# Performance work log

Hardware: AMD Instinct MI355X
Metric: run time of the kernel (lower is better)

## Reference

```python
import jax, jax.numpy as jnp
import numpy as np

# Flax OptimizedLSTMCell gate order: i, f, g, o

def _lstm_step(c, h, x, W_ih, W_hh, b):
    z = x @ W_ih + h @ W_hh + b          # [B, 4H]
    i, f, g, o = jnp.split(z, 4, axis=-1)
    i = jax.nn.sigmoid(i)
    f = jax.nn.sigmoid(f)
    g = jnp.tanh(g)
    o = jax.nn.sigmoid(o)
    c = f * c + i * g
    h = o * jnp.tanh(c)
    return c, h


def setup_inputs() -> dict:
    key = jax.random.key(0)
    ks = jax.random.split(key, 5)
    B, Tw, Ta, F_AUTO, O, H = 1024, 512, 512, 24, 8, 256
    F = F_AUTO + O  # warmup feature dim must equal auto features + output dim
    return {
        "c0": jnp.zeros((B, H), jnp.float32),
        "h0": jnp.zeros((B, H), jnp.float32),
        "warmup_input": jax.random.normal(ks[0], (B, Tw, F), jnp.float32),
        "auto_input": jax.random.normal(ks[1], (B, Ta, F_AUTO), jnp.float32),
        "W_ih": jax.random.normal(ks[2], (F, 4 * H), jnp.float32) * (1.0 / np.sqrt(F)),
        "W_hh": jax.random.normal(ks[3], (H, 4 * H), jnp.float32) * (1.0 / np.sqrt(H)),
        "b": jnp.zeros((4 * H,), jnp.float32),
        "W_out": jax.random.normal(ks[4], (H, O), jnp.float32) * (1.0 / np.sqrt(H)),
        "b_out": jnp.zeros((O,), jnp.float32),
    }


def reference(c0, h0, warmup_input, auto_input, W_ih, W_hh, b, W_out, b_out):
    # ---- warmup phase: plain LSTM scan over warmup_input ----
    def warm_step(carry, x_t):
        c, h = carry
        c, h = _lstm_step(c, h, x_t, W_ih, W_hh, b)
        return (c, h), h

    xs_w = jnp.swapaxes(warmup_input, 0, 1)            # [Tw, B, F] time-major
    (c, h), hs = jax.lax.scan(warm_step, (c0, h0), xs_w)
    warm_h = jnp.swapaxes(hs, 0, 1)                    # [B, Tw, H]
    output_warm = warm_h @ W_out + b_out               # [B, Tw, O]
    y_last = output_warm[:, -1]                        # [B, O]

    def auto_step(carry, x_t):
        c, h, y = carry
        in_x = jnp.concatenate([x_t, y], axis=-1)      # [B, F_auto + O] == [B, F]
        c, h = _lstm_step(c, h, in_x, W_ih, W_hh, b)
        y = h @ W_out + b_out
        return (c, h, y), y

    xs_a = jnp.swapaxes(auto_input, 0, 1)              # [Ta, B, F_auto]
    _, ys = jax.lax.scan(auto_step, (c, h, y_last), xs_a)
    rest_output = jnp.swapaxes(ys, 0, 1)               # [B, Ta, O]

    return jnp.concatenate([output_warm, rest_output], axis=-2)  # [B, Tw+Ta, O]
```

## Files before the change

kernel.cpp:

```cpp
#include <hip/hip_runtime.h>
#include <stdint.h>


#define B_TOTAL   1024
#define H_DIM     256
#define F_WARM    32
#define F_AUTO    24
#define O_DIM     8
#define T_WARM    512
#define T_TOTAL   1024
#define N4H       1024
#define A_STR     104

typedef __attribute__((ext_vector_type(8))) short short8;
typedef __attribute__((ext_vector_type(4))) float float4v;

#define GLOBAL_AS __attribute__((address_space(1)))
#define LDS_AS    __attribute__((address_space(3)))
#define XSCOPE    __HIP_MEMORY_SCOPE_AGENT

__device__ __forceinline__ short f2bf(float x) {
    union { float f; uint32_t u; } v; v.f = x;
    uint32_t r = v.u + 0x7FFFu + ((v.u >> 16) & 1u);
    return (short)(r >> 16);
}
__device__ __forceinline__ float sigmoid_(float x) {
    const float e = __expf(-x);
    return __builtin_amdgcn_rcpf(1.0f + e);
}
__device__ __forceinline__ float tanh_(float x) {
    const float e = __expf(-2.0f * fabsf(x));
    const float t = (1.0f - e) * __builtin_amdgcn_rcpf(1.0f + e);
    return x >= 0.0f ? t : -t;
}
__device__ __forceinline__ uint32_t uc_ld(const uint32_t* p) {
    return __hip_atomic_load(p, __ATOMIC_RELAXED, XSCOPE);
}
__device__ __forceinline__ void uc_st(uint32_t* p, uint32_t v) {
    __hip_atomic_store(p, v, __ATOMIC_RELAXED, XSCOPE);
}

__global__ __launch_bounds__(256, 1)
void lstm_q4(const float* __restrict__ c0, const float* __restrict__ h0,
             const float* __restrict__ warm, const float* __restrict__ autoin,
             const float* __restrict__ W_ih, const float* __restrict__ W_hh,
             const float* __restrict__ bvec, const float* __restrict__ W_out,
             const float* __restrict__ b_out, float* __restrict__ out,
             unsigned short* __restrict__ ws)
{
    const int tid  = threadIdx.x;
    const int w    = tid >> 6;
    const int l    = tid & 63;
    const int n16  = l & 15;
    const int kg   = l >> 4;
    const int bid  = blockIdx.x;
    const int tile = bid & 63;
    const int q    = bid >> 6;
    const int row0 = tile * 16;
    const int hcol = q * 64 + w * 16 + n16;
    const int cl   = w * 16 + n16;

    const int pb0 = ((q + 1) & 3) * 64 + tile;
    const int pb1 = ((q + 2) & 3) * 64 + tile;
    const int pb2 = ((q + 3) & 3) * 64 + tile;

    uint32_t* myflag = (uint32_t*)((char*)ws + (size_t)bid * 64);
    const uint32_t* pf0 = (const uint32_t*)((char*)ws + (size_t)pb0 * 64);
    const uint32_t* pf1 = (const uint32_t*)((char*)ws + (size_t)pb1 * 64);
    const uint32_t* pf2 = (const uint32_t*)((char*)ws + (size_t)pb2 * 64);
    uint32_t* xbase = (uint32_t*)((char*)ws + 16384);
    uint32_t*       obuf = xbase + (size_t)bid * 1024;
    const uint32_t* pd0  = xbase + (size_t)pb0 * 1024;
    const uint32_t* pd1  = xbase + (size_t)pb1 * 1024;
    const uint32_t* pd2  = xbase + (size_t)pb2 * 1024;

    __shared__ __align__(16) short Abuf[2][16 * A_STR];
    __shared__ __align__(16) unsigned short wsWl[4096];
    __shared__ float biasL[256];
    __shared__ __align__(16) float xstage[512];

    for (int idx = tid; idx < 4096; idx += 256) {
        const int i = idx & 7, lane = (idx >> 3) & 63, kk = idx >> 9;
        const int k = kk * 32 + (lane >> 4) * 8 + i;
        const int n = lane & 15;
        wsWl[idx] = (unsigned short)((n < O_DIM) ? f2bf(W_out[k * O_DIM + n]) : (short)0);
    }
    {
        const int g = tid >> 6, loc = tid & 63;
        biasL[tid] = bvec[g * 256 + q * 64 + loc];
    }

    short8 bwx[4];
    short8 bwo[2][4];
    short8 bwhp[3][2][4];
    #pragma unroll
    for (int g = 0; g < 4; ++g) {
        const int col = g * 256 + hcol;
        {
            short8 f;
            #pragma unroll
            for (int i = 0; i < 8; ++i)
                f[i] = f2bf(W_ih[(kg * 8 + i) * N4H + col]);
            bwx[g] = f;
        }
        #pragma unroll
        for (int lc = 0; lc < 2; ++lc) {
            short8 f;
            #pragma unroll
            for (int i = 0; i < 8; ++i)
                f[i] = f2bf(W_hh[(q * 64 + lc * 32 + kg * 8 + i) * N4H + col]);
            bwo[lc][g] = f;
        }
        #pragma unroll
        for (int pi = 0; pi < 3; ++pi) {
            const int qq = (q + 1 + pi) & 3;
            #pragma unroll
            for (int lc = 0; lc < 2; ++lc) {
                short8 f;
                #pragma unroll
                for (int i = 0; i < 8; ++i)
                    f[i] = f2bf(W_hh[(qq * 64 + lc * 32 + kg * 8 + i) * N4H + col]);
                bwhp[pi][lc][g] = f;
            }
        }
    }

    const float bout = (w == 0 && n16 < O_DIM) ? b_out[n16] : 0.0f;

    float creg[4];
    #pragma unroll
    for (int r = 0; r < 4; ++r)
        creg[r] = c0[(size_t)(row0 + kg * 4 + r) * H_DIM + hcol];

    #pragma unroll
    for (int e = 0; e < 2; ++e) {
        const int idx = tid + e * 256;
        const int r = idx >> 5, cx = idx & 31;
        Abuf[0][r * A_STR + cx] =
            f2bf(warm[(size_t)(row0 + r) * (T_WARM * F_WARM) + cx]);
    }
    #pragma unroll
    for (int e = 0; e < 4; ++e) {
        const int idx = tid + e * 256;
        const int r = idx >> 6, c = idx & 63;
        Abuf[0][r * A_STR + F_WARM + c] =
            f2bf(h0[(size_t)(row0 + r) * H_DIM + q * 64 + c]);
    }
    short8 phf[3][2];
    #pragma unroll
    for (int pi = 0; pi < 3; ++pi) {
        const int qq = (q + 1 + pi) & 3;
        #pragma unroll
        for (int lc = 0; lc < 2; ++lc) {
            short8 f;
            #pragma unroll
            for (int i = 0; i < 8; ++i)
                f[i] = f2bf(h0[(size_t)(row0 + n16) * H_DIM
                               + qq * 64 + lc * 32 + kg * 8 + i]);
            phf[pi][lc] = f;
        }
    }

    __syncthreads();
    float bb[4];
    #pragma unroll
    for (int g = 0; g < 4; ++g) bb[g] = biasL[g * 64 + cl];

    const int aoff = n16 * A_STR + kg * 8;
    short* curp = &Abuf[0][0];
    short* nxtp = &Abuf[1][0];
    const short8* wsW8 = (const short8*)wsWl;
    const int shx = (n16 & 1) * 16;

    for (int t = 0; t < T_TOTAL; ++t) {
        __syncthreads();

        if (tid == 0)
            uc_st(myflag, (uint32_t)t);

        uint32_t fv0 = 0, fv1 = 0, fv2 = 0;
        if (t >= 1) { fv0 = uc_ld(pf0); fv1 = uc_ld(pf1); fv2 = uc_ld(pf2); }

        const int tn = t + 1;
        if (tn < T_TOTAL) {
            #pragma unroll
            for (int e = 0; e < 2; ++e) {
                const int idx = tid + e * 256;
                const int r = idx >> 5, cx = idx & 31;
                const float* gp;
                if (tn < T_WARM)
                    gp = &warm[(size_t)(row0 + r) * (T_WARM * F_WARM)
                               + (size_t)tn * F_WARM + cx];
                else
                    gp = &autoin[(size_t)(row0 + r) * (T_WARM * F_AUTO)
                                 + (size_t)(tn - T_WARM) * F_AUTO
                                 + ((cx < F_AUTO) ? cx : 0)];
                __builtin_amdgcn_global_load_lds(
                    (const GLOBAL_AS void*)gp,
                    (LDS_AS void*)&xstage[e * 256 + w * 64], 4, 0, 0);
            }
        }

        const short* ab = curp + aoff;
        short8 afh[2];
        #pragma unroll
        for (int lc = 0; lc < 2; ++lc)
            afh[lc] = *(const short8*)(ab + 32 + lc * 32);

        float4v acc[4];
        #pragma unroll
        for (int g = 0; g < 4; ++g)
            acc[g] = (float4v){0.f, 0.f, 0.f, 0.f};
        #pragma unroll
        for (int lc = 0; lc < 2; ++lc)
            #pragma unroll
            for (int g = 0; g < 4; ++g)
                acc[g] = __builtin_amdgcn_mfma_f32_16x16x32_bf16(
                             afh[lc], bwo[lc][g], acc[g], 0, 0, 0);

        if (t < T_WARM) {
            const short8 af = *(const short8*)(ab);
            #pragma unroll
            for (int g = 0; g < 4; ++g)
                acc[g] = __builtin_amdgcn_mfma_f32_16x16x32_bf16(
                             af, bwx[g], acc[g], 0, 0, 0);
        }

        if (t >= 1) {
            const uint32_t want = (uint32_t)t;
            while (fv0 < want || fv1 < want || fv2 < want) {
                __builtin_amdgcn_s_sleep(1);
                fv0 = uc_ld(pf0); fv1 = uc_ld(pf1); fv2 = uc_ld(pf2);
            }
            asm volatile("" ::: "memory");
            const int slot = ((t - 1) & 1) * 512;
            #pragma unroll
            for (int pi = 0; pi < 3; ++pi) {
                const uint32_t* pd = (pi == 0) ? pd0 : (pi == 1) ? pd1 : pd2;
                #pragma unroll
                for (int lc = 0; lc < 2; ++lc) {
                    uint32_t wv[8];
                    #pragma unroll
                    for (int i = 0; i < 8; ++i)
                        wv[i] = uc_ld(&pd[slot + (lc * 32 + kg * 8 + i) * 8 + (n16 >> 1)]);
                    short8 f;
                    #pragma unroll
                    for (int i = 0; i < 8; ++i)
                        f[i] = (short)((wv[i] >> shx) & 0xFFFFu);
                    phf[pi][lc] = f;
                }
            }
        }

        #pragma unroll
        for (int pi = 0; pi < 3; ++pi)
            #pragma unroll
            for (int lc = 0; lc < 2; ++lc)
                #pragma unroll
                for (int g = 0; g < 4; ++g)
                    acc[g] = __builtin_amdgcn_mfma_f32_16x16x32_bf16(
                                 phf[pi][lc], bwhp[pi][lc][g], acc[g], 0, 0, 0);

        if (w == 0 && t >= 1 && (q == 0 || t >= T_WARM)) {
            float4v ya = (float4v){bout, bout, bout, bout};
            #pragma unroll
            for (int lc = 0; lc < 2; ++lc)
                ya = __builtin_amdgcn_mfma_f32_16x16x32_bf16(
                         afh[lc], wsW8[(q * 2 + lc) * 64 + l], ya, 0, 0, 0);
            #pragma unroll
            for (int pi = 0; pi < 3; ++pi) {
                const int qq = (q + 1 + pi) & 3;
                #pragma unroll
                for (int lc = 0; lc < 2; ++lc)
                    ya = __builtin_amdgcn_mfma_f32_16x16x32_bf16(
                             phf[pi][lc], wsW8[(qq * 2 + lc) * 64 + l], ya, 0, 0, 0);
            }
            if (n16 < O_DIM) {
                if (q == 0) {
                    #pragma unroll
                    for (int r = 0; r < 4; ++r)
                        out[(size_t)(row0 + kg * 4 + r) * (T_TOTAL * O_DIM)
                            + (size_t)(t - 1) * O_DIM + n16] = ya[r];
                }
                if (t >= T_WARM) {
                    #pragma unroll
                    for (int r = 0; r < 4; ++r)
                        curp[(kg * 4 + r) * A_STR + F_AUTO + n16] = f2bf(ya[r]);
                }
            }
        }

        if (t >= T_WARM) {
            __syncthreads();
            const short8 af = *(const short8*)(ab);
            #pragma unroll
            for (int g = 0; g < 4; ++g)
                acc[g] = __builtin_amdgcn_mfma_f32_16x16x32_bf16(
                             af, bwx[g], acc[g], 0, 0, 0);
        }

        uint32_t hp[2];
        {
            float hv0, hv1, hv2, hv3;
            #pragma unroll
            for (int r = 0; r < 4; ++r) {
                const float ig = sigmoid_(acc[0][r] + bb[0]);
                const float fg = sigmoid_(acc[1][r] + bb[1]);
                const float gg = tanh_(acc[2][r] + bb[2]);
                const float og = sigmoid_(acc[3][r] + bb[3]);
                const float cc = fg * creg[r] + ig * gg;
                creg[r] = cc;
                const float hh = og * tanh_(cc);
                if (r == 0) hv0 = hh; else if (r == 1) hv1 = hh;
                else if (r == 2) hv2 = hh; else hv3 = hh;
            }
            uint32_t u0, u1;
            asm("v_cvt_pk_bf16_f32 %0, %1, %2" : "=v"(u0) : "v"(hv0), "v"(hv1));
            asm("v_cvt_pk_bf16_f32 %0, %1, %2" : "=v"(u1) : "v"(hv2), "v"(hv3));
            hp[0] = u0; hp[1] = u1;
        }

        asm volatile("s_waitcnt vmcnt(0)" ::: "memory");

        if (tn < T_TOTAL) {
            #pragma unroll
            for (int e = 0; e < 2; ++e) {
                const int idx = tid + e * 256;
                const int r = idx >> 5, cx = idx & 31;
                if (tn < T_WARM || cx < F_AUTO)
                    nxtp[r * A_STR + cx] = f2bf(xstage[idx]);
            }
        }

        {
            uint32_t* ob = obuf + (t & 1) * 512;
            uc_st(&ob[cl * 8 + kg * 2 + 0], hp[0]);
            uc_st(&ob[cl * 8 + kg * 2 + 1], hp[1]);
        }

        {
            const int ac = F_WARM + cl;
            nxtp[(kg * 4 + 0) * A_STR + ac] = (short)(hp[0] & 0xFFFF);
            nxtp[(kg * 4 + 1) * A_STR + ac] = (short)(hp[0] >> 16);
            nxtp[(kg * 4 + 2) * A_STR + ac] = (short)(hp[1] & 0xFFFF);
            nxtp[(kg * 4 + 3) * A_STR + ac] = (short)(hp[1] >> 16);
        }

        { short* tswap = curp; curp = nxtp; nxtp = tswap; }
    }

    __syncthreads();
    if (tid == 0)
        uc_st(myflag, (uint32_t)T_TOTAL);
    if (q == 0 && w == 0) {
        const uint32_t want = (uint32_t)T_TOTAL;
        uint32_t fv0 = uc_ld(pf0), fv1 = uc_ld(pf1), fv2 = uc_ld(pf2);
        while (fv0 < want || fv1 < want || fv2 < want) {
            __builtin_amdgcn_s_sleep(1);
            fv0 = uc_ld(pf0); fv1 = uc_ld(pf1); fv2 = uc_ld(pf2);
        }
        asm volatile("" ::: "memory");
        const int slot = ((T_TOTAL - 1) & 1) * 512;
        #pragma unroll
        for (int pi = 0; pi < 3; ++pi) {
            const uint32_t* pd = (pi == 0) ? pd0 : (pi == 1) ? pd1 : pd2;
            #pragma unroll
            for (int lc = 0; lc < 2; ++lc) {
                uint32_t wv[8];
                #pragma unroll
                for (int i = 0; i < 8; ++i)
                    wv[i] = uc_ld(&pd[slot + (lc * 32 + kg * 8 + i) * 8 + (n16 >> 1)]);
                short8 f;
                #pragma unroll
                for (int i = 0; i < 8; ++i)
                    f[i] = (short)((wv[i] >> shx) & 0xFFFFu);
                phf[pi][lc] = f;
            }
        }
        const short* ab = curp + aoff;
        float4v ya = (float4v){bout, bout, bout, bout};
        #pragma unroll
        for (int lc = 0; lc < 2; ++lc)
            ya = __builtin_amdgcn_mfma_f32_16x16x32_bf16(
                     *(const short8*)(ab + 32 + lc * 32),
                     wsW8[(0 * 2 + lc) * 64 + l], ya, 0, 0, 0);
        #pragma unroll
        for (int pi = 0; pi < 3; ++pi) {
            const int qq = (0 + 1 + pi) & 3;
            #pragma unroll
            for (int lc = 0; lc < 2; ++lc)
                ya = __builtin_amdgcn_mfma_f32_16x16x32_bf16(
                         phf[pi][lc], wsW8[(qq * 2 + lc) * 64 + l], ya, 0, 0, 0);
        }
        if (n16 < O_DIM) {
            #pragma unroll
            for (int r = 0; r < 4; ++r)
                out[(size_t)(row0 + kg * 4 + r) * (T_TOTAL * O_DIM)
                    + (size_t)(T_TOTAL - 1) * O_DIM + n16] = ya[r];
        }
    }
}

extern "C" void kernel_launch(void* const* d_in, const int* in_sizes, int n_in,
                              void* d_out, int out_size, void* d_ws, size_t ws_size,
                              hipStream_t stream) {
    (void)in_sizes; (void)n_in; (void)out_size; (void)ws_size;
    const float* c0   = (const float*)d_in[0];
    const float* h0   = (const float*)d_in[1];
    const float* warm = (const float*)d_in[2];
    const float* aut  = (const float*)d_in[3];
    const float* Wih  = (const float*)d_in[4];
    const float* Whh  = (const float*)d_in[5];
    const float* b    = (const float*)d_in[6];
    const float* Wout = (const float*)d_in[7];
    const float* bout = (const float*)d_in[8];
    float* out = (float*)d_out;
    unsigned short* ws = (unsigned short*)d_ws;
    hipMemsetAsync(d_ws, 0, 16384, stream);
    hipLaunchKernelGGL(lstm_q4, dim3(256), dim3(256), 0, stream,
                       c0, h0, warm, aut, Wih, Whh, b, Wout, bout, out, ws);
}
```

Baseline: 3.637 ms.

## Compute output projection redundantly per wave and drop block barrier in auto phase

Every wave in the autoregressive phase now computes the y = h·W_out projection itself and passes its bf16 result to the next input MFMA through a small per-wave LDS slot, using only a wave barrier. This removes the block-wide __syncthreads that used to wait for wave 0's projection before the input matmul. The exchange buffer layout is also transposed so each lane can gather its peer h slice with four 64-bit atomic loads plus byte permutes, instead of eight 32-bit loads with shifts. The cost is redundant projection MFMAs on all waves and blocks, and a tighter dependence on the new buffer layout being consistent between writers and readers.

```diff
diff --git a/kernel.cpp b/kernel.cpp
--- a/kernel.cpp
+++ b/kernel.cpp
@@ -38,6 +38,18 @@
 }
 __device__ __forceinline__ void uc_st(uint32_t* p, uint32_t v) {
     __hip_atomic_store(p, v, __ATOMIC_RELAXED, XSCOPE);
+}
+__device__ __forceinline__ short8 ld_slice(const uint32_t* pd, int lc, int kg,
+                                           int n16, uint32_t psel) {
+    const uint64_t* p64 =
+        (const uint64_t*)(pd + (n16 >> 1) * 64 + lc * 32 + kg * 8);
+    union { uint32_t d[4]; short8 s; } u;
+    #pragma unroll
+    for (int j = 0; j < 4; ++j) {
+        const uint64_t wv = __hip_atomic_load(p64 + j, __ATOMIC_RELAXED, XSCOPE);
+        u.d[j] = __builtin_amdgcn_perm((uint32_t)(wv >> 32), (uint32_t)wv, psel);
+    }
+    return u.s;
 }
 
 __global__ __launch_bounds__(256, 1)
@@ -59,6 +71,7 @@
     const int row0 = tile * 16;
     const int hcol = q * 64 + w * 16 + n16;
     const int cl   = w * 16 + n16;
+    const uint32_t psel = 0x05040100u + ((n16 & 1) ? 0x02020202u : 0u);
 
     const int pb0 = ((q + 1) & 3) * 64 + tile;
     const int pb1 = ((q + 2) & 3) * 64 + tile;
@@ -78,6 +91,7 @@
     __shared__ __align__(16) unsigned short wsWl[4096];
     __shared__ float biasL[256];
     __shared__ __align__(16) float xstage[512];
+    __shared__ __align__(16) short ylds[4][128];
 
     for (int idx = tid; idx < 4096; idx += 256) {
         const int i = idx & 7, lane = (idx >> 3) & 63, kk = idx >> 9;
@@ -125,7 +139,7 @@
         }
     }
 
-    const float bout = (w == 0 && n16 < O_DIM) ? b_out[n16] : 0.0f;
+    const float bout = (n16 < O_DIM) ? b_out[n16] : 0.0f;
 
     float creg[4];
     #pragma unroll
@@ -170,7 +184,6 @@
     short* curp = &Abuf[0][0];
     short* nxtp = &Abuf[1][0];
     const short8* wsW8 = (const short8*)wsWl;
-    const int shx = (n16 & 1) * 16;
 
     for (int t = 0; t < T_TOTAL; ++t) {
         __syncthreads();
@@ -236,19 +249,11 @@
             const int slot = ((t - 1) & 1) * 512;
             #pragma unroll
             for (int pi = 0; pi < 3; ++pi) {
-                const uint32_t* pd = (pi == 0) ? pd0 : (pi == 1) ? pd1 : pd2;
+                const uint32_t* pd =
+                    ((pi == 0) ? pd0 : (pi == 1) ? pd1 : pd2) + slot;
                 #pragma unroll
-                for (int lc = 0; lc < 2; ++lc) {
-                    uint32_t wv[8];
-                    #pragma unroll
-                    for (int i = 0; i < 8; ++i)
-                        wv[i] = uc_ld(&pd[slot + (lc * 32 + kg * 8 + i) * 8 + (n16 >> 1)]);
-                    short8 f;
-                    #pragma unroll
-                    for (int i = 0; i < 8; ++i)
-                        f[i] = (short)((wv[i] >> shx) & 0xFFFFu);
-                    phf[pi][lc] = f;
-                }
+                for (int lc = 0; lc < 2; ++lc)
+                    phf[pi][lc] = ld_slice(pd, lc, kg, n16, psel);
             }
         }
 
@@ -261,38 +266,47 @@
                     acc[g] = __builtin_amdgcn_mfma_f32_16x16x32_bf16(
                                  phf[pi][lc], bwhp[pi][lc][g], acc[g], 0, 0, 0);
 
-        if (w == 0 && t >= 1 && (q == 0 || t >= T_WARM)) {
-            float4v ya = (float4v){bout, bout, bout, bout};
-            #pragma unroll
-            for (int lc = 0; lc < 2; ++lc)
-                ya = __builtin_amdgcn_mfma_f32_16x16x32_bf16(
-                         afh[lc], wsW8[(q * 2 + lc) * 64 + l], ya, 0, 0, 0);
-            #pragma unroll
-            for (int pi = 0; pi < 3; ++pi) {
-                const int qq = (q + 1 + pi) & 3;
+        if (t >= 1 && (t >= T_WARM || (q == 0 && w == 0))) {
+            if (t >= T_WARM || (q == 0 && w == 0)) {
+                float4v ya = (float4v){bout, bout, bout, bout};
                 #pragma unroll
                 for (int lc = 0; lc < 2; ++lc)
                     ya = __builtin_amdgcn_mfma_f32_16x16x32_bf16(
-                             phf[pi][lc], wsW8[(qq * 2 + lc) * 64 + l], ya, 0, 0, 0);
-            }
-            if (n16 < O_DIM) {
-                if (q == 0) {
+                             afh[lc], wsW8[(q * 2 + lc) * 64 + l], ya, 0, 0, 0);
+                #pragma unroll
+                for (int pi = 0; pi < 3; ++pi) {
+                    const int qq = (q + 1 + pi) & 3;
+                    #pragma unroll
+                    for (int lc = 0; lc < 2; ++lc)
+                        ya = __builtin_amdgcn_mfma_f32_16x16x32_bf16(
+                                 phf[pi][lc], wsW8[(qq * 2 + lc) * 64 + l], ya, 0, 0, 0);
+                }
+                if (q == 0 && w == 0 && n16 < O_DIM) {
                     #pragma unroll
                     for (int r = 0; r < 4; ++r)
                         out[(size_t)(row0 + kg * 4 + r) * (T_TOTAL * O_DIM)
                             + (size_t)(t - 1) * O_DIM + n16] = ya[r];
                 }
                 if (t >= T_WARM) {
-                    #pragma unroll
-                    for (int r = 0; r < 4; ++r)
-                        curp[(kg * 4 + r) * A_STR + F_AUTO + n16] = f2bf(ya[r]);
+                    uint32_t yp0, yp1;
+                    asm("v_cvt_pk_bf16_f32 %0, %1, %2" : "=v"(yp0) : "v"(ya[0]), "v"(ya[1]));
+                    asm("v_cvt_pk_bf16_f32 %0, %1, %2" : "=v"(yp1) : "v"(ya[2]), "v"(ya[3]));
+                    if (n16 < O_DIM) {
+                        short* yl = &ylds[w][0];
+                        yl[(kg * 4 + 0) * 8 + n16] = (short)(yp0 & 0xFFFF);
+                        yl[(kg * 4 + 1) * 8 + n16] = (short)(yp0 >> 16);
+                        yl[(kg * 4 + 2) * 8 + n16] = (short)(yp1 & 0xFFFF);
+                        yl[(kg * 4 + 3) * 8 + n16] = (short)(yp1 >> 16);
+                    }
+                    __builtin_amdgcn_wave_barrier();
                 }
             }
         }
 
         if (t >= T_WARM) {
-            __syncthreads();
-            const short8 af = *(const short8*)(ab);
+            short8 af;
+            if (kg == 3) af = *(const short8*)&ylds[w][n16 * 8];
+            else         af = *(const short8*)(ab);
             #pragma unroll
             for (int g = 0; g < 4; ++g)
                 acc[g] = __builtin_amdgcn_mfma_f32_16x16x32_bf16(
@@ -334,8 +348,8 @@
 
         {
             uint32_t* ob = obuf + (t & 1) * 512;
-            uc_st(&ob[cl * 8 + kg * 2 + 0], hp[0]);
-            uc_st(&ob[cl * 8 + kg * 2 + 1], hp[1]);
+            uc_st(&ob[(kg * 2 + 0) * 64 + cl], hp[0]);
+            uc_st(&ob[(kg * 2 + 1) * 64 + cl], hp[1]);
         }
 
         {
@@ -363,19 +377,10 @@
         const int slot = ((T_TOTAL - 1) & 1) * 512;
         #pragma unroll
         for (int pi = 0; pi < 3; ++pi) {
-            const uint32_t* pd = (pi == 0) ? pd0 : (pi == 1) ? pd1 : pd2;
-            #pragma unroll
-            for (int lc = 0; lc < 2; ++lc) {
-                uint32_t wv[8];
-                #pragma unroll
-                for (int i = 0; i < 8; ++i)
-                    wv[i] = uc_ld(&pd[slot + (lc * 32 + kg * 8 + i) * 8 + (n16 >> 1)]);
-                short8 f;
-                #pragma unroll
-                for (int i = 0; i < 8; ++i)
-                    f[i] = (short)((wv[i] >> shx) & 0xFFFFu);
-                phf[pi][lc] = f;
-            }
+            const uint32_t* pd = ((pi == 0) ? pd0 : (pi == 1) ? pd1 : pd2) + slot;
+            #pragma unroll
+            for (int lc = 0; lc < 2; ++lc)
+                phf[pi][lc] = ld_slice(pd, lc, kg, n16, psel);
         }
         const short* ab = curp + aoff;
         float4v ya = (float4v){bout, bout, bout, bout};
```

Result: slower. 4.334 ms (+19.2%).

## Use per-wave flags and per-wave output feedback to drop block barrier

Applied to the files above, without the earlier changes.

Each wave now publishes its own progress flag right after storing its slice of h, and consumers wait on the minimum of the four wave flags of each peer block. Previously a single block flag was written at the start of the next step. In the autoregressive phase every wave computes the output projection itself and reads its feedback through a small per-wave LDS buffer, which removes the block-wide __syncthreads between producing y and the input matmul. This shortens the cross-block dependency chain. The cost is redundant y computation in every wave and four times as many flag loads per poll.

```diff
diff --git a/kernel.cpp b/kernel.cpp
--- a/kernel.cpp
+++ b/kernel.cpp
@@ -38,6 +38,14 @@
 }
 __device__ __forceinline__ void uc_st(uint32_t* p, uint32_t v) {
     __hip_atomic_store(p, v, __ATOMIC_RELAXED, XSCOPE);
+}
+__device__ __forceinline__ uint32_t umin_(uint32_t a, uint32_t b) {
+    return a < b ? a : b;
+}
+__device__ __forceinline__ uint32_t flg4(const uint32_t* b) {
+    const uint32_t a = uc_ld(b), c = uc_ld(b + 16);
+    const uint32_t d = uc_ld(b + 32), e = uc_ld(b + 48);
+    return umin_(umin_(a, c), umin_(d, e));
 }
 
 __global__ __launch_bounds__(256, 1)
@@ -64,11 +72,11 @@
     const int pb1 = ((q + 2) & 3) * 64 + tile;
     const int pb2 = ((q + 3) & 3) * 64 + tile;
 
-    uint32_t* myflag = (uint32_t*)((char*)ws + (size_t)bid * 64);
-    const uint32_t* pf0 = (const uint32_t*)((char*)ws + (size_t)pb0 * 64);
-    const uint32_t* pf1 = (const uint32_t*)((char*)ws + (size_t)pb1 * 64);
-    const uint32_t* pf2 = (const uint32_t*)((char*)ws + (size_t)pb2 * 64);
-    uint32_t* xbase = (uint32_t*)((char*)ws + 16384);
+    uint32_t* myflag = (uint32_t*)((char*)ws + ((size_t)bid * 4 + w) * 64);
+    const uint32_t* pf0b = (const uint32_t*)((char*)ws + (size_t)pb0 * 256);
+    const uint32_t* pf1b = (const uint32_t*)((char*)ws + (size_t)pb1 * 256);
+    const uint32_t* pf2b = (const uint32_t*)((char*)ws + (size_t)pb2 * 256);
+    uint32_t* xbase = (uint32_t*)((char*)ws + 65536);
     uint32_t*       obuf = xbase + (size_t)bid * 1024;
     const uint32_t* pd0  = xbase + (size_t)pb0 * 1024;
     const uint32_t* pd1  = xbase + (size_t)pb1 * 1024;
@@ -78,6 +86,7 @@
     __shared__ __align__(16) unsigned short wsWl[4096];
     __shared__ float biasL[256];
     __shared__ __align__(16) float xstage[512];
+    __shared__ __align__(16) short ylds[4][128];
 
     for (int idx = tid; idx < 4096; idx += 256) {
         const int i = idx & 7, lane = (idx >> 3) & 63, kk = idx >> 9;
@@ -125,7 +134,7 @@
         }
     }
 
-    const float bout = (w == 0 && n16 < O_DIM) ? b_out[n16] : 0.0f;
+    const float bout = (n16 < O_DIM) ? b_out[n16] : 0.0f;
 
     float creg[4];
     #pragma unroll
@@ -175,11 +184,8 @@
     for (int t = 0; t < T_TOTAL; ++t) {
         __syncthreads();
 
-        if (tid == 0)
-            uc_st(myflag, (uint32_t)t);
-
-        uint32_t fv0 = 0, fv1 = 0, fv2 = 0;
-        if (t >= 1) { fv0 = uc_ld(pf0); fv1 = uc_ld(pf1); fv2 = uc_ld(pf2); }
+        uint32_t fm0 = 0, fm1 = 0, fm2 = 0;
+        if (t >= 1) { fm0 = flg4(pf0b); fm1 = flg4(pf1b); fm2 = flg4(pf2b); }
 
         const int tn = t + 1;
         if (tn < T_TOTAL) {
@@ -228,9 +234,9 @@
 
         if (t >= 1) {
             const uint32_t want = (uint32_t)t;
-            while (fv0 < want || fv1 < want || fv2 < want) {
+            while (fm0 < want || fm1 < want || fm2 < want) {
                 __builtin_amdgcn_s_sleep(1);
-                fv0 = uc_ld(pf0); fv1 = uc_ld(pf1); fv2 = uc_ld(pf2);
+                fm0 = flg4(pf0b); fm1 = flg4(pf1b); fm2 = flg4(pf2b);
             }
             asm volatile("" ::: "memory");
             const int slot = ((t - 1) & 1) * 512;
@@ -261,7 +267,7 @@
                     acc[g] = __builtin_amdgcn_mfma_f32_16x16x32_bf16(
                                  phf[pi][lc], bwhp[pi][lc][g], acc[g], 0, 0, 0);
 
-        if (w == 0 && t >= 1 && (q == 0 || t >= T_WARM)) {
+        if (t >= 1 && (t >= T_WARM || (q == 0 && w == 0))) {
             float4v ya = (float4v){bout, bout, bout, bout};
             #pragma unroll
             for (int lc = 0; lc < 2; ++lc)
@@ -275,24 +281,31 @@
                     ya = __builtin_amdgcn_mfma_f32_16x16x32_bf16(
                              phf[pi][lc], wsW8[(qq * 2 + lc) * 64 + l], ya, 0, 0, 0);
             }
-            if (n16 < O_DIM) {
-                if (q == 0) {
-                    #pragma unroll
-                    for (int r = 0; r < 4; ++r)
-                        out[(size_t)(row0 + kg * 4 + r) * (T_TOTAL * O_DIM)
-                            + (size_t)(t - 1) * O_DIM + n16] = ya[r];
+            if (q == 0 && w == 0 && n16 < O_DIM) {
+                #pragma unroll
+                for (int r = 0; r < 4; ++r)
+                    out[(size_t)(row0 + kg * 4 + r) * (T_TOTAL * O_DIM)
+                        + (size_t)(t - 1) * O_DIM + n16] = ya[r];
+            }
+            if (t >= T_WARM) {
+                uint32_t yp0, yp1;
+                asm("v_cvt_pk_bf16_f32 %0, %1, %2" : "=v"(yp0) : "v"(ya[0]), "v"(ya[1]));
+                asm("v_cvt_pk_bf16_f32 %0, %1, %2" : "=v"(yp1) : "v"(ya[2]), "v"(ya[3]));
+                if (n16 < O_DIM) {
+                    short* yl = &ylds[w][0];
+                    yl[(kg * 4 + 0) * 8 + n16] = (short)(yp0 & 0xFFFF);
+                    yl[(kg * 4 + 1) * 8 + n16] = (short)(yp0 >> 16);
+                    yl[(kg * 4 + 2) * 8 + n16] = (short)(yp1 & 0xFFFF);
+                    yl[(kg * 4 + 3) * 8 + n16] = (short)(yp1 >> 16);
                 }
-                if (t >= T_WARM) {
-                    #pragma unroll
-                    for (int r = 0; r < 4; ++r)
-                        curp[(kg * 4 + r) * A_STR + F_AUTO + n16] = f2bf(ya[r]);
-                }
+                __builtin_amdgcn_wave_barrier();
             }
         }
 
         if (t >= T_WARM) {
-            __syncthreads();
-            const short8 af = *(const short8*)(ab);
+            short8 af;
+            if (kg == 3) af = *(const short8*)&ylds[w][n16 * 8];
+            else         af = *(const short8*)(ab);
             #pragma unroll
             for (int g = 0; g < 4; ++g)
                 acc[g] = __builtin_amdgcn_mfma_f32_16x16x32_bf16(
@@ -320,7 +333,14 @@
             hp[0] = u0; hp[1] = u1;
         }
 
+        {
+            uint32_t* ob = obuf + (t & 1) * 512;
+            uc_st(&ob[cl * 8 + kg * 2 + 0], hp[0]);
+            uc_st(&ob[cl * 8 + kg * 2 + 1], hp[1]);
+        }
         asm volatile("s_waitcnt vmcnt(0)" ::: "memory");
+        if (l == 0)
+            uc_st(myflag, (uint32_t)(t + 1));
 
         if (tn < T_TOTAL) {
             #pragma unroll
@@ -330,12 +350,6 @@
                 if (tn < T_WARM || cx < F_AUTO)
                     nxtp[r * A_STR + cx] = f2bf(xstage[idx]);
             }
-        }
-
-        {
-            uint32_t* ob = obuf + (t & 1) * 512;
-            uc_st(&ob[cl * 8 + kg * 2 + 0], hp[0]);
-            uc_st(&ob[cl * 8 + kg * 2 + 1], hp[1]);
         }
 
         {
@@ -350,14 +364,12 @@
     }
 
     __syncthreads();
-    if (tid == 0)
-        uc_st(myflag, (uint32_t)T_TOTAL);
     if (q == 0 && w == 0) {
         const uint32_t want = (uint32_t)T_TOTAL;
-        uint32_t fv0 = uc_ld(pf0), fv1 = uc_ld(pf1), fv2 = uc_ld(pf2);
-        while (fv0 < want || fv1 < want || fv2 < want) {
+        uint32_t fm0 = flg4(pf0b), fm1 = flg4(pf1b), fm2 = flg4(pf2b);
+        while (fm0 < want || fm1 < want || fm2 < want) {
             __builtin_amdgcn_s_sleep(1);
-            fv0 = uc_ld(pf0); fv1 = uc_ld(pf1); fv2 = uc_ld(pf2);
+            fm0 = flg4(pf0b); fm1 = flg4(pf1b); fm2 = flg4(pf2b);
         }
         asm volatile("" ::: "memory");
         const int slot = ((T_TOTAL - 1) & 1) * 512;
@@ -416,7 +428,7 @@
     const float* bout = (const float*)d_in[8];
     float* out = (float*)d_out;
     unsigned short* ws = (unsigned short*)d_ws;
-    hipMemsetAsync(d_ws, 0, 16384, stream);
+    hipMemsetAsync(d_ws, 0, 65536, stream);
     hipLaunchKernelGGL(lstm_q4, dim3(256), dim3(256), 0, stream,
                        c0, h0, warm, aut, Wih, Whh, b, Wout, bout, out, ws);
 }
```

Measured after the change: 4.394 ms. 20.8% more time.
